# Optimization experiments

Measured on AMD Instinct MI355X. Metric: run time of the kernel, lower is better.

The kernel has to match this reference:

```python
import jax, jax.numpy as jnp
import numpy as np

B, T, C, H = 8, 2048, 1024, 64
SCALE = H ** -0.5


def setup_inputs() -> dict:
    key = jax.random.key(0)
    kx, kq, kk, kv = jax.random.split(key, 4)
    x = jax.random.normal(kx, (B, T, C), dtype=jnp.float32)
    w_q = jax.random.normal(kq, (C, H), dtype=jnp.float32) * (C ** -0.5)
    w_k = jax.random.normal(kk, (C, H), dtype=jnp.float32) * (C ** -0.5)
    w_v = jax.random.normal(kv, (C, H), dtype=jnp.float32) * (C ** -0.5)
    return {"x": x, "w_q": w_q, "w_k": w_k, "w_v": w_v}


def reference(x, w_q, w_k, w_v):
    # Projections: [B,T,C] @ [C,H] -> [B,T,H]
    q = jnp.einsum('btc,ch->bth', x, w_q)
    k = jnp.einsum('btc,ch->bth', x, w_k)
    v = jnp.einsum('btc,ch->bth', x, w_v)
    # Scaled scores [B,T,T], causal mask, softmax (dropout p=0 -> identity)
    wei = jnp.einsum('bqh,bkh->bqk', q, k) * SCALE
    tq = x.shape[1]
    causal = jnp.tril(jnp.ones((tq, tq), dtype=bool))
    wei = jnp.where(causal[None, :, :], wei, -jnp.inf)
    wei = jax.nn.softmax(wei, axis=-1)
    out = jnp.einsum('bqk,bkh->bqh', wei, v)
    return out
```

## Files before the change

### kernel.cpp

```cpp
#include <hip/hip_runtime.h>
#include <hip/hip_bf16.h>
#include <cstdint>

#define TB 8
#define TT 2048
#define TC 1024
#define TH 64

typedef __bf16 bf16;
typedef __bf16 bf16x2 __attribute__((ext_vector_type(2)));
typedef __bf16 bf16x4 __attribute__((ext_vector_type(4)));
typedef __bf16 bf16x8 __attribute__((ext_vector_type(8)));
typedef float  f32x4  __attribute__((ext_vector_type(4)));

constexpr float QSCALE = 0.125f * 1.44269504088896340736f;

__device__ __forceinline__ void gll16(const void* g, void* l) {
    __builtin_amdgcn_global_load_lds((const __attribute__((address_space(1))) unsigned int*)g,
                                     (__attribute__((address_space(3))) unsigned int*)l, 16, 0, 0);
}

#define WAIT_VM0()   __builtin_amdgcn_s_waitcnt(0x0F70)
#define WAIT_VM5()   __builtin_amdgcn_s_waitcnt(0x0F75)
#define WAIT_LGKM0() __builtin_amdgcn_s_waitcnt(0xC07F)

__global__ void prep_wT(const float* __restrict__ wq, const float* __restrict__ wk,
                        const float* __restrict__ wv, bf16* __restrict__ wT) {
    int idx = blockIdx.x * blockDim.x + threadIdx.x;
    if (idx >= 3 * TH * TC) return;
    int wsel = idx / (TH * TC);
    int rem  = idx % (TH * TC);
    int c = rem / TH;
    int h = rem % TH;
    const float* w = (wsel == 0) ? wq : (wsel == 1) ? wk : wv;
    wT[(size_t)wsel * TH * TC + (size_t)h * TC + c] = (bf16)w[(size_t)c * TH + h];
}

__launch_bounds__(512)
__global__ void proj(const float* __restrict__ x, const bf16* __restrict__ wT,
                     bf16* __restrict__ Q, bf16* __restrict__ K, bf16* __restrict__ VT) {
    __shared__ __align__(16) char lds[122880];
    const int tid  = threadIdx.x;
    const int wv8  = tid >> 6;
    const int lane = tid & 63;
    const int quad = lane >> 4, l16 = lane & 15;
    const int rg   = wv8 & 3;
    const int ch   = wv8 >> 2;
    const int m0   = blockIdx.x * 64;

    const float* xb = x + (size_t)m0 * TC;

    f32x4 acc[6];
#pragma unroll
    for (int g = 0; g < 6; g++) acc[g] = f32x4{0.f, 0.f, 0.f, 0.f};

    const int lr16 = lane >> 4, lc16 = lane & 15;
    const int lr8  = lane >> 3, lc8  = lane & 7;

#define STAGE(kc, bb)                                                          \
    {                                                                          \
        _Pragma("unroll")                                                      \
        for (int i = 0; i < 2; i++) {            \
            int base_row = wv8 * 8 + i * 4;                                    \
            int row = base_row + lr16;                                         \
            int c = lc16 ^ (row & 15);                                         \
            gll16(xb + (size_t)row * TC + (kc) * 64 + c * 4,                   \
                  lds + (bb) * 40960 + base_row * 256);                        \
        }                                                                      \
        _Pragma("unroll")                                                      \
        for (int j = 0; j < 3; j++) {            \
            int idx = wv8 * 3 + j;                                             \
            int w = idx >> 3;                                                  \
            int base_col = (idx & 7) * 8;                                      \
            int col = base_col + lr8;                                          \
            int c = lc8 ^ (col & 7);                                           \
            gll16(wT + (size_t)w * TH * TC + (size_t)col * TC + (kc) * 64 + c * 8, \
                  lds + (bb) * 40960 + 16384 + (w * 64 + base_col) * 128);     \
        }                                                                      \
    }

    STAGE(0, 0);
    STAGE(1, 1);
    for (int kc = 0; kc < 16; kc++) {
        const int cur = kc % 3;
        if (kc < 15) WAIT_VM5(); else WAIT_VM0();
        __builtin_amdgcn_s_barrier();
        __builtin_amdgcn_sched_barrier(0);
        if (kc + 2 < 16) STAGE(kc + 2, (kc + 2) % 3);
        const char* Xb = lds + cur * 40960;
        const char* Wb = lds + cur * 40960 + 16384;
        const int row = rg * 16 + l16;
#pragma unroll
        for (int s = 0; s < 2; s++) {
            int c1 = (s * 8 + 2 * quad) ^ l16;
            int c2 = (s * 8 + 2 * quad + 1) ^ l16;
            f32x4 a0 = *(const f32x4*)(Xb + row * 256 + c1 * 16);
            f32x4 a1 = *(const f32x4*)(Xb + row * 256 + c2 * 16);
            bf16x8 af;
            af[0] = (bf16)a0[0]; af[1] = (bf16)a0[1]; af[2] = (bf16)a0[2]; af[3] = (bf16)a0[3];
            af[4] = (bf16)a1[0]; af[5] = (bf16)a1[1]; af[6] = (bf16)a1[2]; af[7] = (bf16)a1[3];
#pragma unroll
            for (int g = 0; g < 6; g++) {
                int cg = ch * 6 + g;
                int w = cg >> 2;
                int col = (cg & 3) * 16 + l16;
                int c = (s * 4 + quad) ^ (col & 7);
                bf16x8 bq = *(const bf16x8*)(Wb + (w * 64 + col) * 128 + c * 16);
                acc[g] = __builtin_amdgcn_mfma_f32_16x16x32_bf16(af, bq, acc[g], 0, 0, 0);
            }
        }
    }

    const int mrow = m0 + rg * 16 + quad * 4;
    const int b = m0 >> 11;
    const int t = mrow & 2047;
#pragma unroll
    for (int g = 0; g < 6; g++) {
        int cg = ch * 6 + g;
        int w = cg >> 2;
        int col = (cg & 3) * 16 + l16;
        if (w == 0) {
#pragma unroll
            for (int r = 0; r < 4; r++)
                Q[(size_t)(mrow + r) * TH + col] = (bf16)(acc[g][r] * QSCALE);
        } else if (w == 1) {
#pragma unroll
            for (int r = 0; r < 4; r++)
                K[(size_t)(mrow + r) * TH + col] = (bf16)acc[g][r];
        } else {
            bf16x4 o;
#pragma unroll
            for (int r = 0; r < 4; r++) o[r] = (bf16)acc[g][r];
            *(bf16x4*)(VT + ((size_t)b * TH + col) * TT + t) = o;
        }
    }
}
#undef STAGE

__device__ __forceinline__ float packbf(float a, float b) {
    union { bf16x2 h; float f; } u;
    u.h[0] = (bf16)a; u.h[1] = (bf16)b;
    return u.f;
}

__launch_bounds__(256, 3)
__global__ void attn(const bf16* __restrict__ Q, const bf16* __restrict__ K,
                     const bf16* __restrict__ VT, float* __restrict__ out) {
    __shared__ __align__(16) char lds[35840];

    const int tid  = threadIdx.x;
    const int wv   = tid >> 6;
    const int lane = tid & 63;
    const int quad = lane >> 4, l16 = lane & 15;
    const int b  = blockIdx.x & 7;
    const int qc = 63 - (blockIdx.x >> 3);
    const int q0 = qc * 32;

    char* Kst = lds + wv * 8192;
    char* Vst = Kst + 4096;

    const bf16* Qb = Q  + (size_t)b * TT * TH;
    const bf16* Kb = K  + (size_t)b * TT * TH;
    const bf16* Vb = VT + (size_t)b * TH * TT;

    bf16x8 bq[2][2];
#pragma unroll
    for (int qg = 0; qg < 2; qg++)
#pragma unroll
        for (int kh = 0; kh < 2; kh++)
            bq[qg][kh] = *(const bf16x8*)(Qb + (size_t)(q0 + qg * 16 + l16) * TH + kh * 32 + quad * 8);

    f32x4 accO[2][4];
#pragma unroll
    for (int qg = 0; qg < 2; qg++)
#pragma unroll
        for (int g = 0; g < 4; g++) accO[qg][g] = f32x4{0.f, 0.f, 0.f, 0.f};
    float lIp[2] = {0.f, 0.f};

    const int r8 = lane >> 3, c8 = lane & 7;
    const int r4 = lane >> 2, c4 = lane & 3;
    const int src1 = (quad & 1) * 32 + l16;
    const int src2 = src1 + 16;

#define STAGEKV(kt_)                                                            \
    {                                                                           \
        const int k0_ = (kt_) * 32;                                             \
        _Pragma("unroll")                                                       \
        for (int i = 0; i < 4; i++) {                                           \
            int t = i * 8 + r8;                                                 \
            gll16(Kb + (size_t)(k0_ + t) * 64 + ((c8 ^ r8) * 8),                \
                  Kst + i * 1024);                                              \
        }                                                                       \
        _Pragma("unroll")                                                       \
        for (int i = 0; i < 4; i++) {                                           \
            int h = i * 16 + r4;                                                \
            gll16(Vb + (size_t)h * TT + k0_ + ((c4 ^ quad) * 8),                \
                  Vst + i * 1024);                                              \
        }                                                                       \
    }

    if (wv <= qc) {
        STAGEKV(wv);
        for (int kt = wv; kt <= qc; kt += 4) {
            WAIT_VM0();

            bf16x8 ka[2][2], bv[4];
#pragma unroll
            for (int g = 0; g < 2; g++) {
                int t = g * 16 + l16;
                const char* kr = Kst + t * 128;
                ka[g][0] = *(const bf16x8*)(kr + (((quad) ^ (t & 7)) << 4));
                ka[g][1] = *(const bf16x8*)(kr + (((4 + quad) ^ (t & 7)) << 4));
            }
#pragma unroll
            for (int g = 0; g < 4; g++) {
                int h = g * 16 + l16;
                bv[g] = *(const bf16x8*)(Vst + h * 64 + ((quad ^ (l16 >> 2)) << 4));
            }
            WAIT_LGKM0();
            if (kt + 4 <= qc) STAGEKV(kt + 4);

            f32x4 s[2][2];
#pragma unroll
            for (int g = 0; g < 2; g++)
#pragma unroll
                for (int qg = 0; qg < 2; qg++) {
                    f32x4 t0 = f32x4{0.f, 0.f, 0.f, 0.f};
                    t0 = __builtin_amdgcn_mfma_f32_16x16x32_bf16(ka[g][0], bq[qg][0], t0, 0, 0, 0);
                    t0 = __builtin_amdgcn_mfma_f32_16x16x32_bf16(ka[g][1], bq[qg][1], t0, 0, 0, 0);
                    s[qg][g] = t0;
                }

            if (kt == qc) {
#pragma unroll
                for (int qg = 0; qg < 2; qg++) {
                    const int ql = qg * 16 + l16;
#pragma unroll
                    for (int g = 0; g < 2; g++)
#pragma unroll
                        for (int r = 0; r < 4; r++)
                            if (g * 16 + quad * 4 + r > ql) s[qg][g][r] = -3.0e38f;
                }
            }

#pragma unroll
            for (int qg = 0; qg < 2; qg++) {
                float rs = 0.f;
#pragma unroll
                for (int g = 0; g < 2; g++)
#pragma unroll
                    for (int r = 0; r < 4; r++) {
                        float p = __builtin_amdgcn_exp2f(s[qg][g][r]);
                        s[qg][g][r] = p;
                        rs += p;
                    }
                lIp[qg] += rs;
            }

#pragma unroll
            for (int qg = 0; qg < 2; qg++) {
                float p00 = packbf(s[qg][0][0], s[qg][0][1]);
                float p01 = packbf(s[qg][0][2], s[qg][0][3]);
                float p10 = packbf(s[qg][1][0], s[qg][1][1]);
                float p11 = packbf(s[qg][1][2], s[qg][1][3]);
                float A0p0 = __shfl(p00, src1), A0p1 = __shfl(p01, src1);
                float B0p0 = __shfl(p00, src2), B0p1 = __shfl(p01, src2);
                float A1p0 = __shfl(p10, src1), A1p1 = __shfl(p11, src1);
                float B1p0 = __shfl(p10, src2), B1p1 = __shfl(p11, src2);
                bool lo = quad < 2;
                union { float4 f; bf16x8 v; } u;
                u.f = make_float4(lo ? A0p0 : A1p0, lo ? A0p1 : A1p1,
                                  lo ? B0p0 : B1p0, lo ? B0p1 : B1p1);
#pragma unroll
                for (int g = 0; g < 4; g++)
                    accO[qg][g] = __builtin_amdgcn_mfma_f32_16x16x32_bf16(u.v, bv[g], accO[qg][g], 0, 0, 0);
            }
        }
    }
#undef STAGEKV

    float lI[2];
#pragma unroll
    for (int qg = 0; qg < 2; qg++) {
        float l = lIp[qg];
        l += __shfl_xor(l, 16);
        l += __shfl_xor(l, 32);
        lI[qg] = l;
    }

    WAIT_VM0();
    __syncthreads();
    float* Omg = (float*)lds;
    float* Lmg = (float*)(lds + 34816);
#pragma unroll
    for (int qg = 0; qg < 2; qg++)
#pragma unroll
        for (int g = 0; g < 4; g++)
#pragma unroll
            for (int r = 0; r < 4; r++)
                Omg[(size_t)(wv * 32 + qg * 16 + quad * 4 + r) * 68 + g * 16 + l16] = accO[qg][g][r];
    if (quad == 0) {
#pragma unroll
        for (int qg = 0; qg < 2; qg++)
            Lmg[wv * 32 + qg * 16 + l16] = lI[qg];
    }
    __syncthreads();

#pragma unroll
    for (int p = 0; p < 2; p++) {
        const int idx = p * 256 + tid;
        const int q = idx >> 4;
        const int hs = (idx & 15) * 4;
        float denom = 0.f, o0 = 0.f, o1 = 0.f, o2 = 0.f, o3 = 0.f;
#pragma unroll
        for (int w = 0; w < 4; w++) {
            denom += Lmg[w * 32 + q];
            const float* op = Omg + (size_t)(w * 32 + q) * 68 + hs;
            o0 += op[0]; o1 += op[1]; o2 += op[2]; o3 += op[3];
        }
        float inv = 1.f / denom;
        *(float4*)(out + ((size_t)b * TT + q0 + q) * TH + hs) =
            make_float4(o0 * inv, o1 * inv, o2 * inv, o3 * inv);
    }
}

extern "C" void kernel_launch(void* const* d_in, const int* in_sizes, int n_in,
                              void* d_out, int out_size, void* d_ws, size_t ws_size,
                              hipStream_t stream) {
    const float* x  = (const float*)d_in[0];
    const float* wq = (const float*)d_in[1];
    const float* wk = (const float*)d_in[2];
    const float* wv = (const float*)d_in[3];

    char* ws = (char*)d_ws;
    bf16*  wT = (bf16*)(ws);
    bf16*  Q  = (bf16*)(ws + 393216);
    bf16*  K  = (bf16*)(ws + 2490368);
    bf16*  VT = (bf16*)(ws + 4587520);
    float* out = (float*)d_out;

    hipLaunchKernelGGL(prep_wT, dim3(768), dim3(256), 0, stream, wq, wk, wv, wT);
    hipLaunchKernelGGL(proj, dim3(256), dim3(512), 0, stream, x, wT, Q, K, VT);
    hipLaunchKernelGGL(attn, dim3(TB * 64), dim3(256), 0, stream, Q, K, VT, out);
}
```

Baseline: 125.5 us.

## Split attention KV range in two per query chunk and merge partials

Each query chunk's causal key range is split into two halves handled by separate blocks, doubling the grid from 512 to 1024 blocks. Partial unnormalized outputs and denominators go to workspace, and a new merge kernel sums them and normalizes. This is meant to improve load balance and occupancy across CUs on the causal triangle. The cost is an extra kernel launch and extra global traffic for the partials. Merging by plain summation relies on the unnormalized partials sharing a fixed max or scale, as the original cross-wave merge apparently does.

```diff
diff --git a/kernel.cpp b/kernel.cpp
--- a/kernel.cpp
+++ b/kernel.cpp
@@ -145,16 +145,24 @@
 
 __launch_bounds__(256, 3)
 __global__ void attn(const bf16* __restrict__ Q, const bf16* __restrict__ K,
-                     const bf16* __restrict__ VT, float* __restrict__ out) {
+                     const bf16* __restrict__ VT,
+                     float* __restrict__ Opart, float* __restrict__ Lpart) {
     __shared__ __align__(16) char lds[35840];
 
     const int tid  = threadIdx.x;
     const int wv   = tid >> 6;
     const int lane = tid & 63;
     const int quad = lane >> 4, l16 = lane & 15;
-    const int b  = blockIdx.x & 7;
-    const int qc = 63 - (blockIdx.x >> 3);
+    const int bidx = blockIdx.x;
+    const int j    = bidx >> 4;
+    const int b    = (bidx >> 1) & 7;
+    const int half = bidx & 1;
+    const int qc = 63 - j;
     const int q0 = qc * 32;
+    const int nk  = qc + 1;
+    const int n0  = (nk + 1) >> 1;
+    const int klo = half ? n0 : 0;
+    const int khi = half ? nk : n0;
 
     char* Kst = lds + wv * 8192;
     char* Vst = Kst + 4096;
@@ -199,9 +207,9 @@
         }                                                                       \
     }
 
-    if (wv <= qc) {
-        STAGEKV(wv);
-        for (int kt = wv; kt <= qc; kt += 4) {
+    if (klo + wv < khi) {
+        STAGEKV(klo + wv);
+        for (int kt = klo + wv; kt < khi; kt += 4) {
             WAIT_VM0();
 
             bf16x8 ka[2][2], bv[4];
@@ -218,7 +226,7 @@
                 bv[g] = *(const bf16x8*)(Vst + h * 64 + ((quad ^ (l16 >> 2)) << 4));
             }
             WAIT_LGKM0();
-            if (kt + 4 <= qc) STAGEKV(kt + 4);
+            if (kt + 4 < khi) STAGEKV(kt + 4);
 
             f32x4 s[2][2];
 #pragma unroll
@@ -318,9 +326,31 @@
             const float* op = Omg + (size_t)(w * 32 + q) * 68 + hs;
             o0 += op[0]; o1 += op[1]; o2 += op[2]; o3 += op[3];
         }
-        float inv = 1.f / denom;
-        *(float4*)(out + ((size_t)b * TT + q0 + q) * TH + hs) =
-            make_float4(o0 * inv, o1 * inv, o2 * inv, o3 * inv);
+        *(float4*)(Opart + (size_t)bidx * 2048 + q * 64 + hs) = make_float4(o0, o1, o2, o3);
+        if ((idx & 15) == 0) Lpart[bidx * 32 + q] = denom;
+    }
+}
+
+__global__ void attn_merge(const float* __restrict__ Opart, const float* __restrict__ Lpart,
+                           float* __restrict__ out) {
+    const int cidx = blockIdx.x;
+    const int head = cidx >> 6;
+    const int qc   = cidx & 63;
+    const int j    = 63 - qc;
+    const int bid0 = (j << 4) | (head << 1);
+    const int bid1 = bid0 | 1;
+    const int tid  = threadIdx.x;
+#pragma unroll
+    for (int p = 0; p < 2; p++) {
+        const int idx = p * 256 + tid;
+        const int q  = idx >> 4;
+        const int hs = (idx & 15) * 4;
+        float4 a = *(const float4*)(Opart + (size_t)bid0 * 2048 + q * 64 + hs);
+        float4 c = *(const float4*)(Opart + (size_t)bid1 * 2048 + q * 64 + hs);
+        float inv = 1.f / (Lpart[bid0 * 32 + q] + Lpart[bid1 * 32 + q]);
+        *(float4*)(out + ((size_t)head * TT + qc * 32 + q) * TH + hs) =
+            make_float4((a.x + c.x) * inv, (a.y + c.y) * inv,
+                        (a.z + c.z) * inv, (a.w + c.w) * inv);
     }
 }
 
@@ -337,9 +367,12 @@
     bf16*  Q  = (bf16*)(ws + 393216);
     bf16*  K  = (bf16*)(ws + 2490368);
     bf16*  VT = (bf16*)(ws + 4587520);
+    float* Opart = (float*)(ws + 6684672);
+    float* Lpart = (float*)(ws + 15073280);
     float* out = (float*)d_out;
 
     hipLaunchKernelGGL(prep_wT, dim3(768), dim3(256), 0, stream, wq, wk, wv, wT);
     hipLaunchKernelGGL(proj, dim3(256), dim3(512), 0, stream, x, wT, Q, K, VT);
-    hipLaunchKernelGGL(attn, dim3(TB * 64), dim3(256), 0, stream, Q, K, VT, out);
-}
+    hipLaunchKernelGGL(attn, dim3(1024), dim3(256), 0, stream, Q, K, VT, Opart, Lpart);
+    hipLaunchKernelGGL(attn_merge, dim3(512), dim3(256), 0, stream, Opart, Lpart, out);
+}
```

Result: slower. 129.7 us (+3.3%).
